# Optimization experiments

Hardware: AMD Instinct MI355X
Metric: run time of the kernel (lower is better)

Reference implementation:

```python
import jax, jax.numpy as jnp
import numpy as np

BIT = 8
QMAX = 2 ** (BIT - 1) - 1   # 127
QMIN = -(2 ** (BIT - 1))    # -128


def _quant_linear(x, W, b, act_sf):
    """HAWQ-style QuantLinear: per-output-channel symmetric 8-bit weights,
    integer GEMM on the (already-quantized) activation grid, dequantized output.
    Returns (out, weight_scaling_factor)."""
    w_sf = jnp.max(jnp.abs(W), axis=1) / QMAX                      # [out]
    w_int = jnp.clip(jnp.round(W / w_sf[:, None]), QMIN, QMAX)     # [out,in]
    x_int = x / act_sf                                             # integer-valued floats
    b_int = jnp.round(b / (w_sf * act_sf))                         # [out]
    out = (jnp.einsum('bsd,od->bso', x_int, w_int) + b_int) * (w_sf * act_sf)
    return out, w_sf


def _quant_act(x):
    """QuantAct: per-tensor symmetric 8-bit requantization."""
    sf = jnp.max(jnp.abs(x)) / QMAX
    xq = jnp.clip(jnp.round(x / sf), QMIN, QMAX) * sf
    return xq, sf


def setup_inputs() -> dict:
    key = jax.random.key(0)
    k = jax.random.split(key, 5)
    B, S, D, H = 256, 196, 384, 1536
    act_scaling_factor = jnp.array([0.05], jnp.float32)
    x = jax.random.normal(k[0], (B, S, D), jnp.float32)
    # input arrives already fake-quantized on the act_scaling_factor grid
    x = jnp.clip(jnp.round(x / act_scaling_factor), QMIN, QMAX) * act_scaling_factor
    W1 = jax.random.normal(k[1], (H, D), jnp.float32) * 0.02
    b1 = jax.random.normal(k[2], (H,), jnp.float32) * 0.02
    W2 = jax.random.normal(k[3], (D, H), jnp.float32) * 0.02
    b2 = jax.random.normal(k[4], (D,), jnp.float32) * 0.02
    return dict(x=x, W1=W1, b1=b1, W2=W2, b2=b2,
                act_scaling_factor=act_scaling_factor)


def reference(x, W1, b1, W2, b2, act_scaling_factor):
    h, _ = _quant_linear(x, W1, b1, act_scaling_factor)
    h = jax.nn.relu(h)
    h, asf1 = _quant_act(h)
    y, _ = _quant_linear(h, W2, b2, asf1)
    y, asf2 = _quant_act(y)
    return y, asf2
```

## Files before the change

### kernel.cpp

```cpp
#include <hip/hip_runtime.h>
#include <hip/hip_bf16.h>
#include <stdint.h>


#define M_TOT 50176
#define D_IN  384
#define H_MID 1536
#define OUT_N (M_TOT * D_IN)
#define NSLOT 256

typedef int v4i __attribute__((ext_vector_type(4)));

__device__ __forceinline__ float clamp_q(float q) {
  return fminf(fmaxf(q, -128.0f), 127.0f);
}

__device__ __forceinline__ float fast_div(float t, float d, float R) {
  const float q1 = t * R;
  const float r  = fmaf(-d, q1, t);
  return fmaf(r, R, q1);
}


__global__ void quant_w_kernel(const float* __restrict__ W, const float* __restrict__ b,
                               int8_t* __restrict__ Wq, float* __restrict__ wsf,
                               int* __restrict__ bint, const float* __restrict__ asf_p,
                               int cols) {
  const int lane = threadIdx.x & 63;
  const int row  = blockIdx.x * 4 + (threadIdx.x >> 6);
  const float* wr = W + (size_t)row * cols;
  float m = 0.f;
  for (int c = lane; c < cols; c += 64) m = fmaxf(m, fabsf(wr[c]));
#pragma unroll
  for (int off = 32; off; off >>= 1) m = fmaxf(m, __shfl_xor(m, off));
  const float sf = m / 127.0f;
  int8_t* qbase = Wq + (size_t)(row >> 4) * 16 * cols + (row & 15) * 16;
  for (int c = lane; c < cols; c += 64)
    qbase[(c >> 4) * 256 + (c & 15)] = (int8_t)clamp_q(rintf(wr[c] / sf));
  if (lane == 0) {
    wsf[row] = sf;
    if (bint) bint[row] = (int)rintf(b[row] / (sf * asf_p[0]));
  }
}

__global__ void quant_x_kernel(const float* __restrict__ x, int8_t* __restrict__ xq,
                               const float* __restrict__ asf_p) {
  const int lane = threadIdx.x & 63;
  const int wid  = threadIdx.x >> 6;
  const float R = 1.0f / asf_p[0];
  const int r  = lane & 15;
  const int kq = lane >> 4;
  const int ntask = (M_TOT / 16) * 6;
  for (int task = blockIdx.x * 4 + wid; task < ntask; task += gridDim.x * 4) {
    const int pan = task / 6;
    const int kcq = task - pan * 6;
    const float* src = x + ((size_t)pan * 16 + r) * D_IN + (kcq * 4 + kq) * 16;
    int out[4];
#pragma unroll
    for (int q4 = 0; q4 < 4; ++q4) {
      float4 v = *(const float4*)(src + q4 * 4);
      unsigned a0 = (unsigned char)(signed char)clamp_q(rintf(v.x * R));
      unsigned a1 = (unsigned char)(signed char)clamp_q(rintf(v.y * R));
      unsigned a2 = (unsigned char)(signed char)clamp_q(rintf(v.z * R));
      unsigned a3 = (unsigned char)(signed char)clamp_q(rintf(v.w * R));
      out[q4] = (int)(a0 | (a1 << 8) | (a2 << 16) | (a3 << 24));
    }
    *(int4*)(xq + (size_t)pan * 6144 + kcq * 1024 + lane * 16) = *(int4*)out;
  }
}

template <int MODE>
__global__ __launch_bounds__(256, 4) void gemm_i8_kernel(
    const int8_t* __restrict__ A, const int8_t* __restrict__ Bm,
    int K, int ntiles_n,
    const float* __restrict__ sfv, const int* __restrict__ bintv,
    const float* __restrict__ bias, const float* __restrict__ asf_p,
    const unsigned* __restrict__ gmax_in,
    float* __restrict__ Cout, int8_t* __restrict__ Cq,
    unsigned* __restrict__ gmax_out) {
  const int tid  = threadIdx.x;
  const int lane = tid & 63;
  const int wid  = tid >> 6;
  const int cpx = gridDim.x >> 3;
  const int wg  = (blockIdx.x & 7) * cpx + (blockIdx.x >> 3);
  const int bn = wg % ntiles_n;
  const int bm = wg / ntiles_n;
  const int l16 = lane & 15;

  const int rbA = bm * 8 + (wid >> 1) * 4;
  const int rbB = bn * 4 + (wid & 1) * 2;
  const int sK  = 16 * K;
  const int8_t* pa = A  + (size_t)rbA * sK + lane * 16;
  const int8_t* pb = Bm + (size_t)rbB * sK + lane * 16;

  v4i acc[4][2] = {};
  const int ksteps = K >> 6;

  v4i a0[4], b0[2], a1[4], b1[2];
#pragma unroll
  for (int i = 0; i < 4; ++i) a0[i] = *(const v4i*)(pa + i * sK);
#pragma unroll
  for (int j = 0; j < 2; ++j) b0[j] = *(const v4i*)(pb + j * sK);

  for (int ks = 0; ks < ksteps; ks += 2) {
#pragma unroll
    for (int i = 0; i < 4; ++i) a1[i] = *(const v4i*)(pa + i * sK + (ks + 1) * 1024);
#pragma unroll
    for (int j = 0; j < 2; ++j) b1[j] = *(const v4i*)(pb + j * sK + (ks + 1) * 1024);
#pragma unroll
    for (int i = 0; i < 4; ++i)
#pragma unroll
      for (int j = 0; j < 2; ++j)
        acc[i][j] = __builtin_amdgcn_mfma_i32_16x16x64_i8(a0[i], b0[j], acc[i][j], 0, 0, 0);
    if (ks + 2 < ksteps) {
#pragma unroll
      for (int i = 0; i < 4; ++i) a0[i] = *(const v4i*)(pa + i * sK + (ks + 2) * 1024);
#pragma unroll
      for (int j = 0; j < 2; ++j) b0[j] = *(const v4i*)(pb + j * sK + (ks + 2) * 1024);
    }
#pragma unroll
    for (int i = 0; i < 4; ++i)
#pragma unroll
      for (int j = 0; j < 2; ++j)
        acc[i][j] = __builtin_amdgcn_mfma_i32_16x16x64_i8(a1[i], b1[j], acc[i][j], 0, 0, 0);
  }

  float sf1 = 0.f;
  if (MODE != 0) {
    float m = fmaxf(fmaxf(__uint_as_float(gmax_in[lane]),
                          __uint_as_float(gmax_in[lane + 64])),
                    fmaxf(__uint_as_float(gmax_in[lane + 128]),
                          __uint_as_float(gmax_in[lane + 192])));
#pragma unroll
    for (int off = 32; off; off >>= 1) m = fmaxf(m, __shfl_xor(m, off));
    sf1 = m / 127.0f;
  }

  const int wm = (wid >> 1) * 64;
  const int wn = (wid & 1) * 32;
  const int r0 = (lane >> 4) * 4;
  float lmax = 0.f;

  if (MODE == 0) {
#pragma unroll
    for (int j = 0; j < 2; ++j) {
      int mi = acc[0][j][0];
#pragma unroll
      for (int i = 0; i < 4; ++i)
#pragma unroll
        for (int r = 0; r < 4; ++r) mi = max(mi, acc[i][j][r]);
      const int col = bn * 64 + wn + j * 16 + l16;
      lmax = fmaxf(lmax, (float)(mi + bintv[col]) * (sfv[col] * asf_p[0]));
    }
  } else if (MODE == 1) {
    const float asf = asf_p[0];
#pragma unroll
    for (int j = 0; j < 2; ++j) {
      const int col = bn * 64 + wn + j * 16 + l16;
      const float ratio = (sfv[col] * asf) / sf1;
      const int bi = bintv[col];
      const size_t cc = (size_t)((bn * 4 + (wid & 1) * 2 + j) << 8);
#pragma unroll
      for (int i = 0; i < 4; ++i) {
        const size_t prow = (size_t)(bm * 8 + (wid >> 1) * 4 + i) * (16 * H_MID);
#pragma unroll
        for (int r = 0; r < 4; ++r) {
          const float f = (float)(acc[i][j][r] + bi);
          const float q = fminf(fmaxf(rintf(f * ratio), 0.f), 127.0f);
          Cq[prow + cc + (size_t)((r0 + r) * 16 + l16)] = (int8_t)q;
        }
      }
    }
  } else {
#pragma unroll
    for (int j = 0; j < 2; ++j) {
      const int col = bn * 64 + wn + j * 16 + l16;
      const float scale = sfv[col] * sf1;
      const int bi = (int)rintf(bias[col] / scale);
      int mi = acc[0][j][0], mn = acc[0][j][0];
#pragma unroll
      for (int i = 0; i < 4; ++i) {
        const int row = bm * 128 + wm + i * 16 + r0;
#pragma unroll
        for (int r = 0; r < 4; ++r) {
          const int a = acc[i][j][r];
          mi = max(mi, a); mn = min(mn, a);
          Cout[(size_t)(row + r) * D_IN + col] = (float)(a + bi) * scale;
        }
      }
      lmax = fmaxf(lmax, fmaxf(fabsf((float)(mi + bi) * scale),
                               fabsf((float)(mn + bi) * scale)));
    }
  }

  if (MODE != 1) {
#pragma unroll
    for (int off = 32; off; off >>= 1) lmax = fmaxf(lmax, __shfl_xor(lmax, off));
    if (lane == 0) atomicMax(&gmax_out[(wg * 4 + wid) & (NSLOT - 1)], __float_as_uint(lmax));
  }
}

__global__ void final_quant_kernel(float* __restrict__ y, const unsigned* __restrict__ slots,
                                   int n4) {
  __shared__ float s_sf;
  const int tid = threadIdx.x;
  if (tid < 64) {
    float m = fmaxf(fmaxf(__uint_as_float(slots[tid]),
                          __uint_as_float(slots[tid + 64])),
                    fmaxf(__uint_as_float(slots[tid + 128]),
                          __uint_as_float(slots[tid + 192])));
#pragma unroll
    for (int off = 32; off; off >>= 1) m = fmaxf(m, __shfl_xor(m, off));
    if (tid == 0) s_sf = m / 127.0f;
  }
  __syncthreads();
  const float asf2 = s_sf;
  const float R = 1.0f / asf2;
  float4* y4 = (float4*)y;
  const int stride = gridDim.x * blockDim.x;
  for (int i = blockIdx.x * blockDim.x + tid; i < n4; i += stride) {
    float4 v = y4[i];
    v.x = clamp_q(rintf(fast_div(v.x, asf2, R))) * asf2;
    v.y = clamp_q(rintf(fast_div(v.y, asf2, R))) * asf2;
    v.z = clamp_q(rintf(fast_div(v.z, asf2, R))) * asf2;
    v.w = clamp_q(rintf(fast_div(v.w, asf2, R))) * asf2;
    y4[i] = v;
  }
  if (blockIdx.x == 0 && tid == 0) y[(size_t)n4 * 4] = asf2;
}

extern "C" void kernel_launch(void* const* d_in, const int* in_sizes, int n_in,
                              void* d_out, int out_size, void* d_ws, size_t ws_size,
                              hipStream_t stream) {
  const float* x   = (const float*)d_in[0];
  const float* W1  = (const float*)d_in[1];
  const float* b1  = (const float*)d_in[2];
  const float* W2  = (const float*)d_in[3];
  const float* b2  = (const float*)d_in[4];
  const float* asf = (const float*)d_in[5];

  char* ws = (char*)d_ws;
  unsigned* gmax1 = (unsigned*)ws;
  unsigned* gmax2 = (unsigned*)(ws + 1024);
  size_t off = 4096;
  int8_t* xq   = (int8_t*)(ws + off); off += (size_t)M_TOT * D_IN;
  int8_t* w1q  = (int8_t*)(ws + off); off += (size_t)H_MID * D_IN;
  float*  w1sf = (float*)(ws + off);  off += (size_t)H_MID * 4;
  int*    b1i  = (int*)(ws + off);    off += (size_t)H_MID * 4;
  int8_t* w2q  = (int8_t*)(ws + off); off += (size_t)D_IN * H_MID;
  float*  w2sf = (float*)(ws + off);  off += (size_t)D_IN * 4;
  off = (off + 255) & ~(size_t)255;
  int8_t* hq   = (int8_t*)(ws + off); off += (size_t)M_TOT * H_MID;

  hipMemsetAsync(d_ws, 0, 4096, stream);

  quant_w_kernel<<<H_MID / 4, 256, 0, stream>>>(W1, b1, w1q, w1sf, b1i, asf, D_IN);
  quant_w_kernel<<<D_IN / 4, 256, 0, stream>>>(W2, nullptr, w2q, w2sf, nullptr, nullptr, H_MID);
  quant_x_kernel<<<2048, 256, 0, stream>>>(x, xq, asf);

  const int g1 = (M_TOT / 128) * (H_MID / 64);
  const int g2 = (M_TOT / 128) * (D_IN / 64);
  gemm_i8_kernel<0><<<g1, 256, 0, stream>>>(
      xq, w1q, D_IN, H_MID / 64, w1sf, b1i, nullptr, asf,
      nullptr, nullptr, nullptr, gmax1);
  gemm_i8_kernel<1><<<g1, 256, 0, stream>>>(
      xq, w1q, D_IN, H_MID / 64, w1sf, b1i, nullptr, asf,
      gmax1, nullptr, hq, nullptr);
  gemm_i8_kernel<2><<<g2, 256, 0, stream>>>(
      hq, w2q, H_MID, D_IN / 64, w2sf, nullptr, b2, nullptr,
      gmax1, (float*)d_out, nullptr, gmax2);
  final_quant_kernel<<<2048, 256, 0, stream>>>((float*)d_out, gmax2, OUT_N / 4);
}
```

Baseline: 233.1 us.

## Stage GEMM tiles through LDS with async global-to-LDS double buffering

Replaces direct per-wave global register loads in the int8 GEMM with global_load_lds into double-buffered shared memory, with explicit vmcnt waits and barriers. Tiles are shared across waves instead of being loaded redundantly. For the first GEMM the operands are swapped, so the weight matrix becomes the 128-row side and the token dimension the 64-column side, and the epilogues are remapped to match. The MODE 1 output now stores packed 4-byte words. The extra LDS use lowers the occupancy hint from 4 to 3 blocks, and adds barrier overhead.

```diff
diff --git a/kernel.cpp b/kernel.cpp
--- a/kernel.cpp
+++ b/kernel.cpp
@@ -19,6 +19,12 @@
   const float q1 = t * R;
   const float r  = fmaf(-d, q1, t);
   return fmaf(r, R, q1);
+}
+
+__device__ __forceinline__ void gld_lds16(const int8_t* g, int8_t* s) {
+  __builtin_amdgcn_global_load_lds((const __attribute__((address_space(1))) void*)g,
+                                   (__attribute__((address_space(3))) void*)s,
+                                   16, 0, 0);
 }
 
 
@@ -70,59 +76,89 @@
 }
 
 template <int MODE>
-__global__ __launch_bounds__(256, 4) void gemm_i8_kernel(
+__global__ __launch_bounds__(256, 3) void gemm_i8_kernel(
     const int8_t* __restrict__ A, const int8_t* __restrict__ Bm,
-    int K, int ntiles_n,
+    int K, int nt_inner,
     const float* __restrict__ sfv, const int* __restrict__ bintv,
     const float* __restrict__ bias, const float* __restrict__ asf_p,
     const unsigned* __restrict__ gmax_in,
     float* __restrict__ Cout, int8_t* __restrict__ Cq,
     unsigned* __restrict__ gmax_out) {
-  const int tid  = threadIdx.x;
-  const int lane = tid & 63;
-  const int wid  = tid >> 6;
+  __shared__ __align__(16) int8_t sA[2][16384];
+  __shared__ __align__(16) int8_t sB[2][8192];
+  const int tid    = threadIdx.x;
+  const int lane   = tid & 63;
+  const int wid    = tid >> 6;
+  const int tid16  = tid * 16;
+  const int lane16 = lane * 16;
+  const int l16    = lane & 15;
+  const int r0     = (lane >> 4) * 4;
   const int cpx = gridDim.x >> 3;
   const int wg  = (blockIdx.x & 7) * cpx + (blockIdx.x >> 3);
-  const int bn = wg % ntiles_n;
-  const int bm = wg / ntiles_n;
-  const int l16 = lane & 15;
-
-  const int rbA = bm * 8 + (wid >> 1) * 4;
-  const int rbB = bn * 4 + (wid & 1) * 2;
-  const int sK  = 16 * K;
-  const int8_t* pa = A  + (size_t)rbA * sK + lane * 16;
-  const int8_t* pb = Bm + (size_t)rbB * sK + lane * 16;
+  const int bm = (MODE == 2) ? (wg / nt_inner) : (wg % nt_inner);
+  const int bn = (MODE == 2) ? (wg % nt_inner) : (wg / nt_inner);
+
+  const int8_t* gA0 = A  + (size_t)(bm * 8) * (16 * K);
+  const int8_t* gB0 = Bm + (size_t)(bn * 4) * (16 * K);
+  int baseA[4], baseB[2];
+#pragma unroll
+  for (int l = 0; l < 4; ++l) {
+    const int f = l * 4096 + tid16;
+    baseA[l] = (f >> 11) * 16 * K + (f & 2047);
+  }
+#pragma unroll
+  for (int l = 0; l < 2; ++l) {
+    const int f = l * 4096 + tid16;
+    baseB[l] = (f >> 11) * 16 * K + (f & 2047);
+  }
+
+  const int ab = (wid >> 1) * 4;
+  const int bb = (wid & 1) * 2;
 
   v4i acc[4][2] = {};
-  const int ksteps = K >> 6;
-
-  v4i a0[4], b0[2], a1[4], b1[2];
-#pragma unroll
-  for (int i = 0; i < 4; ++i) a0[i] = *(const v4i*)(pa + i * sK);
-#pragma unroll
-  for (int j = 0; j < 2; ++j) b0[j] = *(const v4i*)(pb + j * sK);
-
-  for (int ks = 0; ks < ksteps; ks += 2) {
-#pragma unroll
-    for (int i = 0; i < 4; ++i) a1[i] = *(const v4i*)(pa + i * sK + (ks + 1) * 1024);
-#pragma unroll
-    for (int j = 0; j < 2; ++j) b1[j] = *(const v4i*)(pb + j * sK + (ks + 1) * 1024);
-#pragma unroll
-    for (int i = 0; i < 4; ++i)
+  const int niter = K >> 7;
+
+#pragma unroll
+  for (int l = 0; l < 4; ++l) gld_lds16(gA0 + baseA[l], &sA[0][l * 4096 + tid16]);
+#pragma unroll
+  for (int l = 0; l < 2; ++l) gld_lds16(gB0 + baseB[l], &sB[0][l * 4096 + tid16]);
+
+  for (int c = 0; c < niter; ++c) {
+    const int buf = c & 1;
+    if (c + 1 < niter) {
+      const int co = (c + 1) * 2048;
+#pragma unroll
+      for (int l = 0; l < 4; ++l)
+        gld_lds16(gA0 + baseA[l] + co, &sA[buf ^ 1][l * 4096 + tid16]);
+#pragma unroll
+      for (int l = 0; l < 2; ++l)
+        gld_lds16(gB0 + baseB[l] + co, &sB[buf ^ 1][l * 4096 + tid16]);
+      asm volatile("s_waitcnt vmcnt(6)" ::: "memory");
+    } else {
+      asm volatile("s_waitcnt vmcnt(0)" ::: "memory");
+    }
+    __builtin_amdgcn_s_barrier();
+    __builtin_amdgcn_sched_barrier(0);
+    v4i af[2][4], bf[2][2];
+#pragma unroll
+    for (int ks = 0; ks < 2; ++ks) {
+#pragma unroll
+      for (int i = 0; i < 4; ++i)
+        af[ks][i] = *(const v4i*)&sA[buf][(ab + i) * 2048 + ks * 1024 + lane16];
 #pragma unroll
       for (int j = 0; j < 2; ++j)
-        acc[i][j] = __builtin_amdgcn_mfma_i32_16x16x64_i8(a0[i], b0[j], acc[i][j], 0, 0, 0);
-    if (ks + 2 < ksteps) {
-#pragma unroll
-      for (int i = 0; i < 4; ++i) a0[i] = *(const v4i*)(pa + i * sK + (ks + 2) * 1024);
-#pragma unroll
-      for (int j = 0; j < 2; ++j) b0[j] = *(const v4i*)(pb + j * sK + (ks + 2) * 1024);
-    }
-#pragma unroll
-    for (int i = 0; i < 4; ++i)
-#pragma unroll
-      for (int j = 0; j < 2; ++j)
-        acc[i][j] = __builtin_amdgcn_mfma_i32_16x16x64_i8(a1[i], b1[j], acc[i][j], 0, 0, 0);
+        bf[ks][j] = *(const v4i*)&sB[buf][(bb + j) * 2048 + ks * 1024 + lane16];
+    }
+#pragma unroll
+    for (int ks = 0; ks < 2; ++ks)
+#pragma unroll
+      for (int i = 0; i < 4; ++i)
+#pragma unroll
+        for (int j = 0; j < 2; ++j)
+          acc[i][j] = __builtin_amdgcn_mfma_i32_16x16x64_i8(af[ks][i], bf[ks][j],
+                                                            acc[i][j], 0, 0, 0);
+    __builtin_amdgcn_sched_barrier(0);
+    __builtin_amdgcn_s_barrier();
   }
 
   float sf1 = 0.f;
@@ -136,56 +172,62 @@
     sf1 = m / 127.0f;
   }
 
-  const int wm = (wid >> 1) * 64;
-  const int wn = (wid & 1) * 32;
-  const int r0 = (lane >> 4) * 4;
   float lmax = 0.f;
-
   if (MODE == 0) {
-#pragma unroll
-    for (int j = 0; j < 2; ++j) {
-      int mi = acc[0][j][0];
-#pragma unroll
-      for (int i = 0; i < 4; ++i)
-#pragma unroll
-        for (int r = 0; r < 4; ++r) mi = max(mi, acc[i][j][r]);
-      const int col = bn * 64 + wn + j * 16 + l16;
-      lmax = fmaxf(lmax, (float)(mi + bintv[col]) * (sfv[col] * asf_p[0]));
+    const float asf = asf_p[0];
+#pragma unroll
+    for (int i = 0; i < 4; ++i) {
+      const int hbase = bm * 128 + (wid >> 1) * 64 + i * 16 + r0;
+#pragma unroll
+      for (int r = 0; r < 4; ++r) {
+        const int mi = max(acc[i][0][r], acc[i][1][r]);
+        const int h  = hbase + r;
+        lmax = fmaxf(lmax, (float)(mi + bintv[h]) * (sfv[h] * asf));
+      }
     }
   } else if (MODE == 1) {
     const float asf = asf_p[0];
+    const float R   = 1.0f / sf1;
+#pragma unroll
+    for (int i = 0; i < 4; ++i) {
+      const int hbase = bm * 128 + (wid >> 1) * 64 + i * 16 + r0;
+      const int htile = bm * 8 + (wid >> 1) * 4 + i;
+      float ratio[4];
+      int bi4[4];
+#pragma unroll
+      for (int r = 0; r < 4; ++r) {
+        const int h = hbase + r;
+        ratio[r] = fast_div(sfv[h] * asf, sf1, R);
+        bi4[r]   = bintv[h];
+      }
+#pragma unroll
+      for (int j = 0; j < 2; ++j) {
+        const int m = bn * 64 + (wid & 1) * 32 + j * 16 + l16;
+        unsigned d = 0;
+#pragma unroll
+        for (int r = 0; r < 4; ++r) {
+          const float f = (float)(acc[i][j][r] + bi4[r]);
+          const int q = (int)fminf(fmaxf(rintf(f * ratio[r]), 0.f), 127.f);
+          d |= (unsigned)q << (8 * r);
+        }
+        *(unsigned*)(Cq + (size_t)(m >> 4) * 24576 + htile * 256 + (m & 15) * 16 + r0) = d;
+      }
+    }
+  } else {
 #pragma unroll
     for (int j = 0; j < 2; ++j) {
-      const int col = bn * 64 + wn + j * 16 + l16;
-      const float ratio = (sfv[col] * asf) / sf1;
-      const int bi = bintv[col];
-      const size_t cc = (size_t)((bn * 4 + (wid & 1) * 2 + j) << 8);
+      const int d = bn * 64 + (wid & 1) * 32 + j * 16 + l16;
+      const float scale = sfv[d] * sf1;
+      const int bi = (int)rintf(bias[d] / scale);
+      int mi = acc[0][j][0], mn = acc[0][j][0];
 #pragma unroll
       for (int i = 0; i < 4; ++i) {
-        const size_t prow = (size_t)(bm * 8 + (wid >> 1) * 4 + i) * (16 * H_MID);
-#pragma unroll
-        for (int r = 0; r < 4; ++r) {
-          const float f = (float)(acc[i][j][r] + bi);
-          const float q = fminf(fmaxf(rintf(f * ratio), 0.f), 127.0f);
-          Cq[prow + cc + (size_t)((r0 + r) * 16 + l16)] = (int8_t)q;
-        }
-      }
-    }
-  } else {
-#pragma unroll
-    for (int j = 0; j < 2; ++j) {
-      const int col = bn * 64 + wn + j * 16 + l16;
-      const float scale = sfv[col] * sf1;
-      const int bi = (int)rintf(bias[col] / scale);
-      int mi = acc[0][j][0], mn = acc[0][j][0];
-#pragma unroll
-      for (int i = 0; i < 4; ++i) {
-        const int row = bm * 128 + wm + i * 16 + r0;
+        const int row = bm * 128 + (wid >> 1) * 64 + i * 16 + r0;
 #pragma unroll
         for (int r = 0; r < 4; ++r) {
           const int a = acc[i][j][r];
           mi = max(mi, a); mn = min(mn, a);
-          Cout[(size_t)(row + r) * D_IN + col] = (float)(a + bi) * scale;
+          Cout[(size_t)(row + r) * D_IN + d] = (float)(a + bi) * scale;
         }
       }
       lmax = fmaxf(lmax, fmaxf(fabsf((float)(mi + bi) * scale),
@@ -258,13 +300,13 @@
   quant_w_kernel<<<D_IN / 4, 256, 0, stream>>>(W2, nullptr, w2q, w2sf, nullptr, nullptr, H_MID);
   quant_x_kernel<<<2048, 256, 0, stream>>>(x, xq, asf);
 
-  const int g1 = (M_TOT / 128) * (H_MID / 64);
+  const int g1 = (H_MID / 128) * (M_TOT / 64);
   const int g2 = (M_TOT / 128) * (D_IN / 64);
   gemm_i8_kernel<0><<<g1, 256, 0, stream>>>(
-      xq, w1q, D_IN, H_MID / 64, w1sf, b1i, nullptr, asf,
+      w1q, xq, D_IN, H_MID / 128, w1sf, b1i, nullptr, asf,
       nullptr, nullptr, nullptr, gmax1);
   gemm_i8_kernel<1><<<g1, 256, 0, stream>>>(
-      xq, w1q, D_IN, H_MID / 64, w1sf, b1i, nullptr, asf,
+      w1q, xq, D_IN, H_MID / 128, w1sf, b1i, nullptr, asf,
       gmax1, nullptr, hq, nullptr);
   gemm_i8_kernel<2><<<g2, 256, 0, stream>>>(
       hq, w2q, H_MID, D_IN / 64, w2sf, nullptr, b2, nullptr,
```

After: 230.6 us. About the same (-1.1%).
